# Kernel tuning notes

Measured on AMD Instinct MI355X. Metric: run time of the kernel, lower is better.

The kernel has to match this reference:

```python
import jax, jax.numpy as jnp
import numpy as np
import math

IN_FEATURES = 512
RFF_FEATURES = 2048
OUT_FEATURES = 1000
N = 8192
RIDGE_PENALTY = 1.0
MEAN_FIELD_FACTOR = 25.0
RFF_SCALAR = math.sqrt(RFF_FEATURES / 2)  # 32.0


def _random_ortho(key, n, m):
    q, _ = jnp.linalg.qr(jax.random.normal(key, (n, m), dtype=jnp.float32))
    return q


def setup_inputs() -> dict:
    key = jax.random.key(0)
    k_d, k_w, k_norm, k_b, k_lw, k_lb, k_cov = jax.random.split(key, 7)
    D = jax.random.normal(k_d, (N, IN_FEATURES), dtype=jnp.float32)
    # RFF weight: concat of random orthonormal blocks (rff_features > in_features)
    ws = []
    dim_left = RFF_FEATURES
    kk = k_w
    while dim_left > IN_FEATURES:
        kk, sub = jax.random.split(kk)
        ws.append(_random_ortho(sub, IN_FEATURES, IN_FEATURES))
        dim_left -= IN_FEATURES
    kk, sub = jax.random.split(kk)
    ws.append(_random_ortho(sub, IN_FEATURES, dim_left))
    W = jnp.concatenate(ws, axis=1)  # [in, rff]
    feature_norm = jax.random.normal(k_norm, W.shape, dtype=jnp.float32) ** 2
    W = W * jnp.sqrt(feature_norm.sum(0))
    b = jax.random.uniform(k_b, (RFF_FEATURES,), dtype=jnp.float32) * (2.0 * math.pi)
    # logit head (nn.Linear): weight [out, rff], bias [out]
    bound = 1.0 / math.sqrt(RFF_FEATURES)
    logit_w = jax.random.uniform(k_lw, (OUT_FEATURES, RFF_FEATURES), dtype=jnp.float32,
                                 minval=-bound, maxval=bound)
    logit_b = jax.random.uniform(k_lb, (OUT_FEATURES,), dtype=jnp.float32,
                                 minval=-bound, maxval=bound)
    # positive-definite covariance buffer (stand-in for inverted precision)
    A = jax.random.normal(k_cov, (RFF_FEATURES, RFF_FEATURES), dtype=jnp.float32) * 0.01
    covariance = A @ A.T + jnp.eye(RFF_FEATURES, dtype=jnp.float32)
    return {"D": D, "W": W, "b": b, "logit_w": logit_w, "logit_b": logit_b,
            "covariance": covariance}


def reference(D, W, b, logit_w, logit_b, covariance):
    # RFF feature map: cos(D @ W + b) / rff_scalar  -> [N, rff]
    Phi = jnp.cos(D @ W + b) / RFF_SCALAR
    # linear head -> [N, out]
    pred = Phi @ logit_w.T + logit_b
    # diag(Phi @ cov @ Phi.T) * ridge computed row-wise in O(N*r^2)
    diag_cov = jnp.sum((Phi @ covariance) * Phi, axis=-1) * RIDGE_PENALTY  # [N]
    logits_scale = jnp.sqrt(1.0 + diag_cov * MEAN_FIELD_FACTOR)
    return pred / logits_scale[:, None]
```

## Files before the change

kernel.cpp:

```cpp
#include <hip/hip_runtime.h>
#include <hip/hip_fp8.h>
#include <math.h>

#define N_ROWS 8192
#define IN_F   512
#define RFF    2048
#define OUT_F  1000
#define OUT_PAD 1024
#define INV_RFF_SCALAR 0.03125f
#define MEAN_FIELD 25.0f

typedef __attribute__((ext_vector_type(8))) short short8;
typedef __attribute__((ext_vector_type(4))) float f32x4;
typedef __attribute__((ext_vector_type(2))) long long2v;

__device__ __forceinline__ unsigned short f32_to_bf16(float f) {
    unsigned u = __float_as_uint(f);
    unsigned r = 0x7FFFu + ((u >> 16) & 1u);
    return (unsigned short)((u + r) >> 16);
}
__device__ __forceinline__ float bf16_to_f32(unsigned short h) {
    return __uint_as_float(((unsigned)h) << 16);
}
__device__ __forceinline__ unsigned char f32_to_fp8(float x) {
    __hip_fp8_e4m3 q(x);
    return (unsigned char)q.__x;
}

__device__ __forceinline__ int perm64(int k) {
    return (k & ~63) | (((k >> 3) & 3) << 4) | (((k >> 5) & 1) << 3) | (k & 7);
}

__device__ __forceinline__ const uint4* gsrc(const unsigned short* X, int ldx,
                                             int r0, int k0, int q) {
    int rt = q >> 6, L = q & 63;
    int r = r0 + rt * 16 + (L & 15);
    int k = k0 + ((L >> 4) << 3);
    return (const uint4*)(X + (size_t)r * ldx + k);
}
__device__ __forceinline__ void stage_tile(const unsigned short* __restrict__ X, int ldx,
                                           int r0, int k0, unsigned short* lds,
                                           int w, int lane) {
    #pragma unroll
    for (int half = 0; half < 2; ++half) {
        int qb = half * 256 + w * 64;
        const uint4* g = gsrc(X, ldx, r0, k0, qb + lane);
        __builtin_amdgcn_global_load_lds(
            (const __attribute__((address_space(1))) void*)g,
            (__attribute__((address_space(3))) void*)(lds + qb * 8),
            16, 0, 0);
    }
}

__device__ __forceinline__ void stage_tile64(const unsigned short* __restrict__ X,
                                             int r0, int k0, unsigned char* lds,
                                             int w, int lane) {
    #pragma unroll
    for (int h = 0; h < 4; ++h) {
        int qb = h * 256 + w * 64;
        int q = qb + lane;
        int rt = q >> 7, c = (q >> 4) & 7, r = q & 15;
        const void* g = X + (size_t)(r0 + rt * 16 + r) * RFF + k0 + c * 8;
        __builtin_amdgcn_global_load_lds(
            (const __attribute__((address_space(1))) void*)g,
            (__attribute__((address_space(3))) void*)(lds + qb * 16),
            16, 0, 0);
    }
}

__device__ __forceinline__ void stage_tile8(const unsigned char* __restrict__ X,
                                            int r0, int k0b, unsigned char* lds,
                                            int w, int lane) {
    #pragma unroll
    for (int h = 0; h < 4; ++h) {
        int qb = h * 256 + w * 64;
        int q = qb + lane;
        int rt = q >> 7, c = (q >> 4) & 7, r = q & 15;
        const void* g = X + (size_t)(r0 + rt * 16 + r) * RFF + k0b + c * 16;
        __builtin_amdgcn_global_load_lds(
            (const __attribute__((address_space(1))) void*)g,
            (__attribute__((address_space(3))) void*)(lds + qb * 16),
            16, 0, 0);
    }
}

__global__ __launch_bounds__(256) void conv_split_kernel(
    const float* __restrict__ X, unsigned short* __restrict__ H,
    unsigned short* __restrict__ L, int n4)
{
    int i = blockIdx.x * 256 + threadIdx.x;
    if (i >= n4) return;
    float4 v = ((const float4*)X)[i];
    ushort4 h, l;
    h.x = f32_to_bf16(v.x); l.x = f32_to_bf16(v.x - bf16_to_f32(h.x));
    h.y = f32_to_bf16(v.y); l.y = f32_to_bf16(v.y - bf16_to_f32(h.y));
    h.z = f32_to_bf16(v.z); l.z = f32_to_bf16(v.z - bf16_to_f32(h.z));
    h.w = f32_to_bf16(v.w); l.w = f32_to_bf16(v.w - bf16_to_f32(h.w));
    ((ushort4*)H)[i] = h;
    ((ushort4*)L)[i] = l;
}

__global__ __launch_bounds__(256) void conv_covu8_kernel(
    const float* __restrict__ X, unsigned char* __restrict__ O)
{
    int i = blockIdx.x * 256 + threadIdx.x;
    int base = i * 4;
    int row = base >> 11;
    int col = base & 2047;
    int bn = row >> 7, bk = col >> 7;
    float w = (bk < bn) ? 16.0f : (bk == bn ? 8.0f : 0.0f);
    float4 v = ((const float4*)X)[i];
    float w0 = (col + 0 == row) ? 0.0f : w;
    float w1 = (col + 1 == row) ? 0.0f : w;
    float w2 = (col + 2 == row) ? 0.0f : w;
    float w3 = (col + 3 == row) ? 0.0f : w;
    uchar4 o;
    o.x = f32_to_fp8(v.x * w0); o.y = f32_to_fp8(v.y * w1);
    o.z = f32_to_fp8(v.z * w2); o.w = f32_to_fp8(v.w * w3);
    *(uchar4*)(O + (size_t)row * RFF + perm64(col)) = o;
}

__global__ __launch_bounds__(256) void conv_covd_kernel(
    const float* __restrict__ X, float* __restrict__ Cd)
{
    int i = blockIdx.x * 256 + threadIdx.x;
    if (i < RFF) Cd[i] = X[(size_t)i * RFF + i];
}

__global__ __launch_bounds__(256) void conv_phi8_kernel(
    const unsigned short* __restrict__ Phi16, unsigned char* __restrict__ Phi8)
{
    int i = blockIdx.x * 256 + threadIdx.x;
    int base = i * 4;
    int row = base >> 11;
    int col = base & 2047;
    ushort4 v = ((const ushort4*)Phi16)[i];
    uchar4 o;
    o.x = f32_to_fp8(bf16_to_f32(v.x) * 32.0f);
    o.y = f32_to_fp8(bf16_to_f32(v.y) * 32.0f);
    o.z = f32_to_fp8(bf16_to_f32(v.z) * 32.0f);
    o.w = f32_to_fp8(bf16_to_f32(v.w) * 32.0f);
    *(uchar4*)(Phi8 + (size_t)row * RFF + perm64(col)) = o;
}

__global__ __launch_bounds__(256) void conv_lw_kernel(
    const float* __restrict__ Lw, unsigned short* __restrict__ O)
{
    int i = blockIdx.x * 256 + threadIdx.x;
    int base = i * 4;
    int row = base >> 11;
    ushort4 o;
    if (row < OUT_F) {
        float4 v = ((const float4*)Lw)[i];
        o.x = f32_to_bf16(v.x); o.y = f32_to_bf16(v.y);
        o.z = f32_to_bf16(v.z); o.w = f32_to_bf16(v.w);
    } else {
        o.x = o.y = o.z = o.w = 0;
    }
    ((ushort4*)O)[i] = o;
}

__global__ __launch_bounds__(256) void conv_wt_kernel(
    const float* __restrict__ W, unsigned short* __restrict__ TH,
    unsigned short* __restrict__ TL)
{
    __shared__ float tile[64][65];
    const int tid = threadIdx.x;
    const int n0 = blockIdx.x * 64;
    const int k0 = blockIdx.y * 64;
    #pragma unroll
    for (int i = 0; i < 16; ++i) {
        int e = i * 256 + tid;
        int r = e >> 6, c = e & 63;
        tile[r][c] = W[(size_t)(k0 + r) * RFF + n0 + c];
    }
    __syncthreads();
    #pragma unroll
    for (int i = 0; i < 16; ++i) {
        int e = i * 256 + tid;
        int r = e >> 6, c = e & 63;
        float v = tile[c][r];
        unsigned short h = f32_to_bf16(v);
        unsigned short l = f32_to_bf16(v - bf16_to_f32(h));
        TH[(size_t)(n0 + r) * IN_F + k0 + c] = h;
        TL[(size_t)(n0 + r) * IN_F + k0 + c] = l;
    }
}

__global__ __launch_bounds__(256) void phi_mfma_kernel(
    const unsigned short* __restrict__ Dh, const unsigned short* __restrict__ Dl,
    const unsigned short* __restrict__ Wth, const unsigned short* __restrict__ Wtl,
    const float* __restrict__ bias, unsigned short* __restrict__ Phi)
{
    __shared__ unsigned short ldsAh[4096], ldsAl[4096], ldsBh[4096], ldsBl[4096];
    const int tid = threadIdx.x;
    const int w = tid >> 6, lane = tid & 63;
    const int wm = w >> 1, wn = w & 1;
    const int r0 = blockIdx.y * 128;
    const int c0 = blockIdx.x * 128;

    f32x4 acc[4][4];
    #pragma unroll
    for (int i = 0; i < 4; ++i)
        #pragma unroll
        for (int j = 0; j < 4; ++j)
            acc[i][j] = (f32x4)(0.0f);

    for (int k0 = 0; k0 < IN_F; k0 += 32) {
        __syncthreads();
        stage_tile(Dh,  IN_F, r0, k0, ldsAh, w, lane);
        stage_tile(Dl,  IN_F, r0, k0, ldsAl, w, lane);
        stage_tile(Wth, IN_F, c0, k0, ldsBh, w, lane);
        stage_tile(Wtl, IN_F, c0, k0, ldsBl, w, lane);
        __syncthreads();

        short8 fah[4], fal[4], fbh[4], fbl[4];
        #pragma unroll
        for (int t = 0; t < 4; ++t) {
            fah[t] = *(const short8*)(ldsAh + ((wm * 4 + t) * 64 + lane) * 8);
            fal[t] = *(const short8*)(ldsAl + ((wm * 4 + t) * 64 + lane) * 8);
            fbh[t] = *(const short8*)(ldsBh + ((wn * 4 + t) * 64 + lane) * 8);
            fbl[t] = *(const short8*)(ldsBl + ((wn * 4 + t) * 64 + lane) * 8);
        }
        #pragma unroll
        for (int mt = 0; mt < 4; ++mt)
            #pragma unroll
            for (int nt = 0; nt < 4; ++nt) {
                acc[mt][nt] = __builtin_amdgcn_mfma_f32_16x16x32_bf16(
                    fah[mt], fbh[nt], acc[mt][nt], 0, 0, 0);
                acc[mt][nt] = __builtin_amdgcn_mfma_f32_16x16x32_bf16(
                    fah[mt], fbl[nt], acc[mt][nt], 0, 0, 0);
                acc[mt][nt] = __builtin_amdgcn_mfma_f32_16x16x32_bf16(
                    fal[mt], fbh[nt], acc[mt][nt], 0, 0, 0);
            }
    }

    const int quad = lane >> 4, ln = lane & 15;
    #pragma unroll
    for (int mt = 0; mt < 4; ++mt)
        #pragma unroll
        for (int nt = 0; nt < 4; ++nt) {
            int col = c0 + wn * 64 + nt * 16 + ln;
            float bv = bias[col];
            #pragma unroll
            for (int reg = 0; reg < 4; ++reg) {
                int row = r0 + wm * 64 + mt * 16 + quad * 4 + reg;
                float z = acc[mt][nt][reg] + bv;
                float p = __cosf(z) * INV_RFF_SCALAR;
                Phi[(size_t)row * RFF + col] = f32_to_bf16(p);
            }
        }
}

__global__ __launch_bounds__(256) void diag8_kernel(
    const unsigned char* __restrict__ Phi8, const unsigned char* __restrict__ CovU8,
    const unsigned short* __restrict__ Phi16, const float* __restrict__ Cd,
    float* __restrict__ diag)
{
    __shared__ __align__(16) unsigned char ldsA[16384];
    __shared__ __align__(16) unsigned char ldsB[16384];
    const int tid = threadIdx.x;
    const int w = tid >> 6, lane = tid & 63;
    const int wm = w >> 1, wn = w & 1;
    const int quad = lane >> 4, ln = lane & 15;
    const int J = 15 - blockIdx.x;
    const int r0 = blockIdx.y * 128;
    const int c0 = J * 128;
    const int kmax = (J + 1) * 128;

    f32x4 acc[4][4];
    #pragma unroll
    for (int i = 0; i < 4; ++i)
        #pragma unroll
        for (int j = 0; j < 4; ++j)
            acc[i][j] = (f32x4)(0.0f);

    for (int k0 = 0; k0 < kmax; k0 += 128) {
        __syncthreads();
        stage_tile8(Phi8,  r0, k0, ldsA, w, lane);
        stage_tile8(CovU8, c0, k0, ldsB, w, lane);
        __syncthreads();

        #pragma unroll
        for (int kb = 0; kb < 2; ++kb) {
            long2v fa[4], fb[4];
            #pragma unroll
            for (int t = 0; t < 4; ++t) {
                fa[t] = *(const long2v*)(ldsA + (((wm * 4 + t) * 128 + (kb * 4 + quad) * 16 + ln) << 4));
                fb[t] = *(const long2v*)(ldsB + (((wn * 4 + t) * 128 + (kb * 4 + quad) * 16 + ln) << 4));
            }
            #pragma unroll
            for (int mt = 0; mt < 4; ++mt)
                #pragma unroll
                for (int nt = 0; nt < 4; ++nt)
                    acc[mt][nt] = __builtin_amdgcn_mfma_f32_16x16x32_fp8_fp8(
                        fa[mt].x, fb[nt].x, acc[mt][nt], 0, 0, 0);
            #pragma unroll
            for (int mt = 0; mt < 4; ++mt)
                #pragma unroll
                for (int nt = 0; nt < 4; ++nt)
                    acc[mt][nt] = __builtin_amdgcn_mfma_f32_16x16x32_fp8_fp8(
                        fa[mt].y, fb[nt].y, acc[mt][nt], 0, 0, 0);
        }
    }

    float cd[4];
    #pragma unroll
    for (int nt = 0; nt < 4; ++nt)
        cd[nt] = 256.0f * Cd[c0 + wn * 64 + nt * 16 + ln];
    #pragma unroll
    for (int mt = 0; mt < 4; ++mt) {
        float psum[4] = {0.f, 0.f, 0.f, 0.f};
        #pragma unroll
        for (int nt = 0; nt < 4; ++nt) {
            int col = c0 + wn * 64 + nt * 16 + ln;
            #pragma unroll
            for (int reg = 0; reg < 4; ++reg) {
                int row = r0 + wm * 64 + mt * 16 + quad * 4 + reg;
                float pv = bf16_to_f32(Phi16[(size_t)row * RFF + col]);
                psum[reg] = fmaf(fmaf(cd[nt], pv, acc[mt][nt][reg]), pv, psum[reg]);
            }
        }
        #pragma unroll
        for (int off = 1; off < 16; off <<= 1)
            #pragma unroll
            for (int reg = 0; reg < 4; ++reg)
                psum[reg] += __shfl_xor(psum[reg], off, 16);
        if (ln == 0) {
            #pragma unroll
            for (int reg = 0; reg < 4; ++reg) {
                int row = r0 + wm * 64 + mt * 16 + quad * 4 + reg;
                atomicAdd(&diag[row], psum[reg] * (1.0f / 256.0f));
            }
        }
    }
}

__global__ __launch_bounds__(256) void pred_mfma_kernel(
    const unsigned short* __restrict__ Phi, const unsigned short* __restrict__ Lw,
    const float* __restrict__ Lb, const float* __restrict__ diag,
    float* __restrict__ out)
{
    __shared__ __align__(16) unsigned char ldsA[16384];
    __shared__ __align__(16) unsigned char ldsB[16384];
    const int tid = threadIdx.x;
    const int w = tid >> 6, lane = tid & 63;
    const int wm = w >> 1, wn = w & 1;
    const int quad = lane >> 4, ln = lane & 15;
    const int r0 = blockIdx.y * 128;
    const int c0 = blockIdx.x * 128;

    f32x4 acc[4][4];
    #pragma unroll
    for (int i = 0; i < 4; ++i)
        #pragma unroll
        for (int j = 0; j < 4; ++j)
            acc[i][j] = (f32x4)(0.0f);

    for (int k0 = 0; k0 < RFF; k0 += 64) {
        __syncthreads();
        stage_tile64(Phi, r0, k0, ldsA, w, lane);
        stage_tile64(Lw,  c0, k0, ldsB, w, lane);
        __syncthreads();

        #pragma unroll
        for (int s = 0; s < 2; ++s) {
            short8 fa[4], fb[4];
            #pragma unroll
            for (int t = 0; t < 4; ++t) {
                fa[t] = *(const short8*)(ldsA + (((wm * 4 + t) * 128 + (s * 4 + quad) * 16 + ln) << 4));
                fb[t] = *(const short8*)(ldsB + (((wn * 4 + t) * 128 + (s * 4 + quad) * 16 + ln) << 4));
            }
            #pragma unroll
            for (int mt = 0; mt < 4; ++mt)
                #pragma unroll
                for (int nt = 0; nt < 4; ++nt)
                    acc[mt][nt] = __builtin_amdgcn_mfma_f32_16x16x32_bf16(
                        fa[mt], fb[nt], acc[mt][nt], 0, 0, 0);
        }
    }

    #pragma unroll
    for (int mt = 0; mt < 4; ++mt) {
        float s[4];
        #pragma unroll
        for (int reg = 0; reg < 4; ++reg) {
            int row = r0 + wm * 64 + mt * 16 + quad * 4 + reg;
            s[reg] = 1.0f / sqrtf(1.0f + MEAN_FIELD * diag[row]);
        }
        #pragma unroll
        for (int nt = 0; nt < 4; ++nt) {
            int col = c0 + wn * 64 + nt * 16 + ln;
            if (col < OUT_F) {
                float bv = Lb[col];
                #pragma unroll
                for (int reg = 0; reg < 4; ++reg) {
                    int row = r0 + wm * 64 + mt * 16 + quad * 4 + reg;
                    out[(size_t)row * OUT_F + col] = (acc[mt][nt][reg] + bv) * s[reg];
                }
            }
        }
    }
}

extern "C" void kernel_launch(void* const* d_in, const int* in_sizes, int n_in,
                              void* d_out, int out_size, void* d_ws, size_t ws_size,
                              hipStream_t stream) {
    const float* D    = (const float*)d_in[0];
    const float* W    = (const float*)d_in[1];
    const float* bias = (const float*)d_in[2];
    const float* Lw   = (const float*)d_in[3];
    const float* Lb   = (const float*)d_in[4];
    const float* cov  = (const float*)d_in[5];
    float* out = (float*)d_out;

    char* p = (char*)d_ws;
    unsigned short* Phi16 = (unsigned short*)p;  p += (size_t)N_ROWS * RFF * 2;
    unsigned char*  Phi8  = (unsigned char*)p;
    unsigned short* Dh    = (unsigned short*)p;  p += (size_t)N_ROWS * IN_F * 2;
    unsigned short* Dl    = (unsigned short*)p;  p += (size_t)N_ROWS * IN_F * 2;
    unsigned short* Wth   = (unsigned short*)p;  p += (size_t)RFF * IN_F * 2;
    unsigned short* Wtl   = (unsigned short*)p;  p += (size_t)RFF * IN_F * 2;
    unsigned short* Lw16  = (unsigned short*)p;  p += (size_t)OUT_PAD * RFF * 2;
    unsigned char*  CovU8 = (unsigned char*)p;
    float*          Cd    = (float*)(p + (size_t)RFF * RFF);
    p += (size_t)RFF * RFF * 2;
    float* diag           = (float*)p;

    hipMemsetAsync(diag, 0, N_ROWS * sizeof(float), stream);

    dim3 blk(256);
    conv_split_kernel<<<dim3((N_ROWS * IN_F / 4 + 255) / 256), blk, 0, stream>>>(D, Dh, Dl, N_ROWS * IN_F / 4);
    conv_wt_kernel<<<dim3(RFF / 64, IN_F / 64), blk, 0, stream>>>(W, Wth, Wtl);
    conv_lw_kernel<<<dim3(OUT_PAD * RFF / 4 / 256), blk, 0, stream>>>(Lw, Lw16);
    conv_covu8_kernel<<<dim3(RFF * RFF / 4 / 256), blk, 0, stream>>>(cov, CovU8);
    conv_covd_kernel<<<dim3(RFF / 256), blk, 0, stream>>>(cov, Cd);

    phi_mfma_kernel<<<dim3(RFF / 128, N_ROWS / 128), blk, 0, stream>>>(Dh, Dl, Wth, Wtl, bias, Phi16);
    conv_phi8_kernel<<<dim3(N_ROWS * RFF / 4 / 256), blk, 0, stream>>>(Phi16, Phi8);

    diag8_kernel<<<dim3(16, N_ROWS / 128), blk, 0, stream>>>(Phi8, CovU8, Phi16, Cd, diag);
    pred_mfma_kernel<<<dim3(OUT_PAD / 128, N_ROWS / 128), blk, 0, stream>>>(Phi16, Lw16, Lb, diag, out);
}
```

Baseline: 321.0 us.

## Rewrite Phi GEMM as 256x256 tile with double-buffered 8-wave pipeline

Replaces the 128x128 Phi GEMM kernel with a 512-thread, 256x256-tile kernel. It concatenates the three split-bf16 products into one K=1536 loop (Dh*Wth, Dh*Wtl, Dl*Wth). Global-to-LDS loads are double-buffered and issued in four interleaved phases with explicit barriers, vmcnt waits and setprio around the MFMA bursts. A block-index swizzle improves L2 reuse. The intent is to hide load latency and raise MFMA utilisation. The cost is much more register and LDS pressure (128 KB LDS, 32 accumulators), and the hand-coded waitcnt ordering is fragile.

```diff
diff --git a/kernel.cpp b/kernel.cpp
--- a/kernel.cpp
+++ b/kernel.cpp
@@ -9,6 +9,7 @@
 #define OUT_PAD 1024
 #define INV_RFF_SCALAR 0.03125f
 #define MEAN_FIELD 25.0f
+#define PHI_NT 24
 
 typedef __attribute__((ext_vector_type(8))) short short8;
 typedef __attribute__((ext_vector_type(4))) float f32x4;
@@ -29,27 +30,6 @@
 
 __device__ __forceinline__ int perm64(int k) {
     return (k & ~63) | (((k >> 3) & 3) << 4) | (((k >> 5) & 1) << 3) | (k & 7);
-}
-
-__device__ __forceinline__ const uint4* gsrc(const unsigned short* X, int ldx,
-                                             int r0, int k0, int q) {
-    int rt = q >> 6, L = q & 63;
-    int r = r0 + rt * 16 + (L & 15);
-    int k = k0 + ((L >> 4) << 3);
-    return (const uint4*)(X + (size_t)r * ldx + k);
-}
-__device__ __forceinline__ void stage_tile(const unsigned short* __restrict__ X, int ldx,
-                                           int r0, int k0, unsigned short* lds,
-                                           int w, int lane) {
-    #pragma unroll
-    for (int half = 0; half < 2; ++half) {
-        int qb = half * 256 + w * 64;
-        const uint4* g = gsrc(X, ldx, r0, k0, qb + lane);
-        __builtin_amdgcn_global_load_lds(
-            (const __attribute__((address_space(1))) void*)g,
-            (__attribute__((address_space(3))) void*)(lds + qb * 8),
-            16, 0, 0);
-    }
 }
 
 __device__ __forceinline__ void stage_tile64(const unsigned short* __restrict__ X,
@@ -187,65 +167,162 @@
     }
 }
 
-__global__ __launch_bounds__(256) void phi_mfma_kernel(
+
+__device__ __forceinline__ void gload16u(const void* g, unsigned short* lds) {
+    __builtin_amdgcn_global_load_lds(
+        (const __attribute__((address_space(1))) void*)g,
+        (__attribute__((address_space(3))) void*)lds, 16, 0, 0);
+}
+
+__device__ __forceinline__ void stageA_g(const unsigned short* __restrict__ src,
+                                         int r0, int kk, unsigned short* ldsbuf,
+                                         int Qa, int h, int w, int lane) {
+    int q   = w * 64 + lane;
+    int RTl = h * 8 + Qa * 4 + (q >> 7);
+    int c   = (q >> 4) & 7, r = q & 15;
+    const void* g = src + (size_t)(r0 + RTl * 16 + r) * IN_F + kk + c * 8;
+    int RTu = h * 8 + Qa * 4 + (w >> 1);
+    int cu  = (w & 1) * 4;
+    gload16u(g, ldsbuf + RTu * 1024 + cu * 128);
+}
+
+__device__ __forceinline__ void stageB_g(const unsigned short* __restrict__ src,
+                                         int cc0, int kk, unsigned short* ldsbuf,
+                                         int nh, int h, int w, int lane) {
+    int q    = w * 64 + lane;
+    int i    = q >> 7;
+    int RTp  = (i >> 1) * 4 + nh * 2 + (i & 1);
+    int c    = (q >> 4) & 7, r = q & 15;
+    const void* g = src + (size_t)(cc0 + h * 128 + RTp * 16 + r) * IN_F + kk + c * 8;
+    int iu   = w >> 1;
+    int RTpu = (iu >> 1) * 4 + nh * 2 + (iu & 1);
+    int RTu  = h * 8 + RTpu;
+    int cu   = (w & 1) * 4;
+    gload16u(g, ldsbuf + RTu * 1024 + cu * 128);
+}
+
+#define BAR() do { asm volatile("" ::: "memory"); \
+                   __builtin_amdgcn_s_barrier();  \
+                   asm volatile("" ::: "memory"); } while (0)
+#define WAITVM(N) asm volatile("s_waitcnt vmcnt(" #N ")" ::: "memory")
+
+#define PHI_PHASE(mh, nh, ...) do {                                            \
+    short8 fa[4][2], fb[2][2];                                                 \
+    _Pragma("unroll")                                                          \
+    for (int i_ = 0; i_ < 4; ++i_) {                                           \
+        fa[i_][0] = *(const short8*)(A + ((wm)*8 + (mh)*4 + i_) * 1024         \
+                                       + quad * 128 + ln * 8);                 \
+        fa[i_][1] = *(const short8*)(A + ((wm)*8 + (mh)*4 + i_) * 1024         \
+                                       + 512 + quad * 128 + ln * 8);           \
+    }                                                                          \
+    _Pragma("unroll")                                                          \
+    for (int j_ = 0; j_ < 2; ++j_) {                                           \
+        fb[j_][0] = *(const short8*)(B + ((wn)*4 + (nh)*2 + j_) * 1024         \
+                                       + quad * 128 + ln * 8);                 \
+        fb[j_][1] = *(const short8*)(B + ((wn)*4 + (nh)*2 + j_) * 1024         \
+                                       + 512 + quad * 128 + ln * 8);           \
+    }                                                                          \
+    __VA_ARGS__;                                                               \
+    BAR();                                                                     \
+    __builtin_amdgcn_s_setprio(1);                                             \
+    _Pragma("unroll")                                                          \
+    for (int s_ = 0; s_ < 2; ++s_)                                             \
+        _Pragma("unroll")                                                      \
+        for (int i_ = 0; i_ < 4; ++i_)                                         \
+            _Pragma("unroll")                                                  \
+            for (int j_ = 0; j_ < 2; ++j_)                                     \
+                acc[(mh)*4 + i_][(nh)*2 + j_] =                                \
+                    __builtin_amdgcn_mfma_f32_16x16x32_bf16(                   \
+                        fa[i_][s_], fb[j_][s_],                                \
+                        acc[(mh)*4 + i_][(nh)*2 + j_], 0, 0, 0);               \
+    __builtin_amdgcn_s_setprio(0);                                             \
+    BAR();                                                                     \
+} while (0)
+
+__global__ __launch_bounds__(512, 2) void phi_mfma8p_kernel(
     const unsigned short* __restrict__ Dh, const unsigned short* __restrict__ Dl,
     const unsigned short* __restrict__ Wth, const unsigned short* __restrict__ Wtl,
     const float* __restrict__ bias, unsigned short* __restrict__ Phi)
 {
-    __shared__ unsigned short ldsAh[4096], ldsAl[4096], ldsBh[4096], ldsBl[4096];
+    __shared__ unsigned short ldsA[2 * 16384];
+    __shared__ unsigned short ldsB[2 * 16384];
     const int tid = threadIdx.x;
     const int w = tid >> 6, lane = tid & 63;
-    const int wm = w >> 1, wn = w & 1;
-    const int r0 = blockIdx.y * 128;
-    const int c0 = blockIdx.x * 128;
-
-    f32x4 acc[4][4];
-    #pragma unroll
-    for (int i = 0; i < 4; ++i)
+    const int wm = w >> 2, wn = w & 3;
+    const int quad = lane >> 4, ln = lane & 15;
+
+    const int bid = blockIdx.x;
+    const int wg = ((bid & 7) << 5) | (bid >> 3);
+    const int r0 = (wg & 31) * 256;
+    const int c0 = (wg >> 5) * 256;
+
+    f32x4 acc[8][4];
+    #pragma unroll
+    for (int i = 0; i < 8; ++i)
         #pragma unroll
         for (int j = 0; j < 4; ++j)
             acc[i][j] = (f32x4)(0.0f);
 
-    for (int k0 = 0; k0 < IN_F; k0 += 32) {
-        __syncthreads();
-        stage_tile(Dh,  IN_F, r0, k0, ldsAh, w, lane);
-        stage_tile(Dl,  IN_F, r0, k0, ldsAl, w, lane);
-        stage_tile(Wth, IN_F, c0, k0, ldsBh, w, lane);
-        stage_tile(Wtl, IN_F, c0, k0, ldsBl, w, lane);
-        __syncthreads();
-
-        short8 fah[4], fal[4], fbh[4], fbl[4];
-        #pragma unroll
-        for (int t = 0; t < 4; ++t) {
-            fah[t] = *(const short8*)(ldsAh + ((wm * 4 + t) * 64 + lane) * 8);
-            fal[t] = *(const short8*)(ldsAl + ((wm * 4 + t) * 64 + lane) * 8);
-            fbh[t] = *(const short8*)(ldsBh + ((wn * 4 + t) * 64 + lane) * 8);
-            fbl[t] = *(const short8*)(ldsBl + ((wn * 4 + t) * 64 + lane) * 8);
-        }
-        #pragma unroll
-        for (int mt = 0; mt < 4; ++mt)
-            #pragma unroll
-            for (int nt = 0; nt < 4; ++nt) {
-                acc[mt][nt] = __builtin_amdgcn_mfma_f32_16x16x32_bf16(
-                    fah[mt], fbh[nt], acc[mt][nt], 0, 0, 0);
-                acc[mt][nt] = __builtin_amdgcn_mfma_f32_16x16x32_bf16(
-                    fah[mt], fbl[nt], acc[mt][nt], 0, 0, 0);
-                acc[mt][nt] = __builtin_amdgcn_mfma_f32_16x16x32_bf16(
-                    fal[mt], fbh[nt], acc[mt][nt], 0, 0, 0);
-            }
-    }
-
-    const int quad = lane >> 4, ln = lane & 15;
-    #pragma unroll
-    for (int mt = 0; mt < 4; ++mt)
+    stageA_g(Dh,  r0, 0, ldsA, 0, 0, w, lane);
+    stageA_g(Dh,  r0, 0, ldsA, 0, 1, w, lane);
+    stageA_g(Dh,  r0, 0, ldsA, 1, 0, w, lane);
+    stageA_g(Dh,  r0, 0, ldsA, 1, 1, w, lane);
+    stageB_g(Wth, c0, 0, ldsB, 0, 0, w, lane);
+    stageB_g(Wth, c0, 0, ldsB, 0, 1, w, lane);
+    stageB_g(Wth, c0, 0, ldsB, 1, 0, w, lane);
+    stageB_g(Wth, c0, 0, ldsB, 1, 1, w, lane);
+    stageA_g(Dh,  r0, 64, ldsA + 16384, 0, 0, w, lane);
+    stageA_g(Dh,  r0, 64, ldsA + 16384, 0, 1, w, lane);
+    stageB_g(Wth, c0, 64, ldsB + 16384, 0, 0, w, lane);
+    stageB_g(Wth, c0, 64, ldsB + 16384, 0, 1, w, lane);
+    WAITVM(4);
+    BAR();
+
+    for (int t = 0; t < PHI_NT; ++t) {
+        const int buf = t & 1;
+        const unsigned short* A = ldsA + buf * 16384;
+        const unsigned short* B = ldsB + buf * 16384;
+        unsigned short* curA = ldsA + buf * 16384;
+        unsigned short* curB = ldsB + buf * 16384;
+        unsigned short* othA = ldsA + (buf ^ 1) * 16384;
+        unsigned short* othB = ldsB + (buf ^ 1) * 16384;
+        const bool has1 = (t + 1) < PHI_NT, has2 = (t + 2) < PHI_NT;
+        const int k1 = (t + 1) * 64, k2 = (t + 2) * 64;
+        const int kk1 = k1 & 511, kk2 = k2 & 511;
+        const unsigned short* A1 = (k1 >= 1024) ? Dl : Dh;
+        const unsigned short* B1 = (k1 >= 1024) ? Wth : (k1 >= 512 ? Wtl : Wth);
+        const unsigned short* A2 = (k2 >= 1024) ? Dl : Dh;
+        const unsigned short* B2 = (k2 >= 1024) ? Wth : (k2 >= 512 ? Wtl : Wth);
+
+        PHI_PHASE(0, 0,
+            if (has1) { stageA_g(A1, r0, kk1, othA, 1, 0, w, lane);
+                        stageA_g(A1, r0, kk1, othA, 1, 1, w, lane); });
+        PHI_PHASE(0, 1,
+            if (has1) { stageB_g(B1, c0, kk1, othB, 1, 0, w, lane);
+                        stageB_g(B1, c0, kk1, othB, 1, 1, w, lane); });
+        PHI_PHASE(1, 0,
+            if (has2) { stageA_g(A2, r0, kk2, curA, 0, 0, w, lane);
+                        stageA_g(A2, r0, kk2, curA, 0, 1, w, lane); });
+        PHI_PHASE(1, 1,
+            if (has2) { stageB_g(B2, c0, kk2, curB, 0, 0, w, lane);
+                        stageB_g(B2, c0, kk2, curB, 0, 1, w, lane);
+                        WAITVM(4); }
+            else if (has1) { WAITVM(0); });
+    }
+
+    float bv[4];
+    #pragma unroll
+    for (int nt = 0; nt < 4; ++nt)
+        bv[nt] = bias[c0 + wn * 64 + nt * 16 + ln];
+    #pragma unroll
+    for (int mt = 0; mt < 8; ++mt)
         #pragma unroll
         for (int nt = 0; nt < 4; ++nt) {
             int col = c0 + wn * 64 + nt * 16 + ln;
-            float bv = bias[col];
             #pragma unroll
             for (int reg = 0; reg < 4; ++reg) {
-                int row = r0 + wm * 64 + mt * 16 + quad * 4 + reg;
-                float z = acc[mt][nt][reg] + bv;
+                int row = r0 + wm * 128 + mt * 16 + quad * 4 + reg;
+                float z = acc[mt][nt][reg] + bv[nt];
                 float p = __cosf(z) * INV_RFF_SCALAR;
                 Phi[(size_t)row * RFF + col] = f32_to_bf16(p);
             }
@@ -436,7 +513,7 @@
     conv_covu8_kernel<<<dim3(RFF * RFF / 4 / 256), blk, 0, stream>>>(cov, CovU8);
     conv_covd_kernel<<<dim3(RFF / 256), blk, 0, stream>>>(cov, Cd);
 
-    phi_mfma_kernel<<<dim3(RFF / 128, N_ROWS / 128), blk, 0, stream>>>(Dh, Dl, Wth, Wtl, bias, Phi16);
+    phi_mfma8p_kernel<<<dim3(256), dim3(512), 0, stream>>>(Dh, Dl, Wth, Wtl, bias, Phi16);
     conv_phi8_kernel<<<dim3(N_ROWS * RFF / 4 / 256), blk, 0, stream>>>(Phi16, Phi8);
 
     diag8_kernel<<<dim3(16, N_ROWS / 128), blk, 0, stream>>>(Phi8, CovU8, Phi16, Cd, diag);
```

Result: slower. 328.4 us (+2.3%).
